# Kernel optimization log

Measured on AMD Instinct MI355X. Metric: run time of the kernel, lower is better.

The kernel has to match this reference:

```python
import jax, jax.numpy as jnp
import numpy as np

ALPHA = 0.2  # LeakyReLU negative slope (init arg alpha)


def setup_inputs() -> dict:
    key = jax.random.key(0)
    k1, k2, k3 = jax.random.split(key, 3)
    B, N, F_in, F_out = 8, 2048, 256, 256
    inp = jax.random.normal(k1, (B, N, F_in), dtype=jnp.float32)
    adj = jnp.ones((B, N, N), dtype=jnp.float32)  # unused by the module's forward
    # xavier_uniform with gain=1.414
    gain = 1.414
    bW = gain * np.sqrt(6.0 / (F_in + F_out))
    W = jax.random.uniform(k2, (F_in, F_out), minval=-bW, maxval=bW, dtype=jnp.float32)
    ba = gain * np.sqrt(6.0 / (2 * F_out + 1))
    a = jax.random.uniform(k3, (2 * F_out, 1), minval=-ba, maxval=ba, dtype=jnp.float32)
    return {"inp": inp, "adj": adj, "W": W, "a": a}


def reference(inp, adj, W, a):
    # inp: [B, N, F_in]; W: [F_in, F_out]; a: [2*F_out, 1]. adj is unused (as in source).
    F_out = W.shape[1]
    h = jnp.matmul(inp, W)  # [B, N, F_out]
    # e[b,i,j] = leakyrelu(a1 . h_i + a2 . h_j)  (equivalent to the repeat+cat+matmul)
    a1 = a[:F_out, 0]
    a2 = a[F_out:, 0]
    s1 = jnp.einsum('bnf,f->bn', h, a1)  # [B, N]
    s2 = jnp.einsum('bnf,f->bn', h, a2)  # [B, N]
    e = jax.nn.leaky_relu(s1[:, :, None] + s2[:, None, :], negative_slope=ALPHA)  # [B, N, N]
    # global per-batch min-max normalization, then affine *30 - 20
    mn = jnp.min(e, axis=(1, 2), keepdims=True)
    mx = jnp.max(e, axis=(1, 2), keepdims=True)
    e = (e - mn) / (mx - mn) * 30.0 - 20.0
    attention = jax.nn.sigmoid(e)  # dropout p=0 / eval: identity
    h_prime = jnp.matmul(attention, h)  # [B, N, F_out]
    h_prime = jax.nn.elu(h_prime)  # concat=True branch
    return h_prime, attention
```

## Files before the change

kernel.cpp:

```cpp
#include <hip/hip_runtime.h>
#include <stdint.h>

#define B_   8
#define N_   2048
#define F_   256
#define BN_  (B_ * N_)
#define ALPHA_ 0.2f

typedef __attribute__((ext_vector_type(8))) short  short8;
typedef __attribute__((ext_vector_type(4))) float  f32x4;

__device__ __forceinline__ unsigned short f2bf(float x) {
  uint32_t u = __float_as_uint(x);
  uint32_t r = (u + 0x7fffu + ((u >> 16) & 1u)) >> 16;
  return (unsigned short)r;
}

__device__ __forceinline__ uint32_t fkey(float f) {
  uint32_t b = __float_as_uint(f);
  return b ^ (uint32_t)(((int32_t)b >> 31) | (int32_t)0x80000000);
}
__device__ __forceinline__ float ikey(uint32_t k) {
  uint32_t b = (k & 0x80000000u) ? (k ^ 0x80000000u) : ~k;
  return __uint_as_float(b);
}

__device__ __forceinline__ void async_load16(const void* g, void* l) {
  __builtin_amdgcn_global_load_lds(
      (const __attribute__((address_space(1))) uint32_t*)g,
      (__attribute__((address_space(3))) uint32_t*)l, 16, 0, 0);
}

__device__ __forceinline__ void nt_store4(float* p, f32x4 v) {
  __builtin_nontemporal_store(v, (f32x4*)p);
}

__global__ void k_cvt_w(const float* __restrict__ W, unsigned short* __restrict__ WT) {
  int k = blockIdx.x, n = threadIdx.x;
  WT[n * F_ + k] = f2bf(W[k * F_ + n]);
}

__launch_bounds__(256, 1)
__global__ void k_gemm1(const float* __restrict__ inp,
                        const unsigned short* __restrict__ WT,
                        const float* __restrict__ avec,
                        unsigned short* __restrict__ hT,
                        float* __restrict__ s1g, float* __restrict__ s2g,
                        uint32_t* __restrict__ maxk, uint32_t* __restrict__ mink) {
  __shared__ __align__(16) unsigned short Atile[64 * 32];
  __shared__ __align__(16) unsigned short Btile[256 * 32];
  __shared__ __align__(16) unsigned short Trans[256 * 72];
  __shared__ float s1_lds[64], s2_lds[64];

  const int tid  = threadIdx.x;
  const int wave = tid >> 6, lane = tid & 63;
  const int n16  = lane & 15, quad = lane >> 4;
  const int i0   = blockIdx.x * 64;
  const int b    = i0 >> 11;

  if (tid < 64) { s1_lds[tid] = 0.0f; s2_lds[tid] = 0.0f; }

  f32x4 acc[4][4];
  #pragma unroll
  for (int mt = 0; mt < 4; ++mt)
    #pragma unroll
    for (int nt = 0; nt < 4; ++nt) acc[mt][nt] = (f32x4){0.f, 0.f, 0.f, 0.f};

  for (int k0 = 0; k0 < F_; k0 += 32) {
    {
      int r = tid >> 2, cp = tid & 3;
      const float* gp = inp + (size_t)(i0 + r) * F_ + k0 + cp * 8;
      float4 va = *(const float4*)gp;
      float4 vb = *(const float4*)(gp + 4);
      short8 sv;
      sv[0] = (short)f2bf(va.x); sv[1] = (short)f2bf(va.y);
      sv[2] = (short)f2bf(va.z); sv[3] = (short)f2bf(va.w);
      sv[4] = (short)f2bf(vb.x); sv[5] = (short)f2bf(vb.y);
      sv[6] = (short)f2bf(vb.z); sv[7] = (short)f2bf(vb.w);
      *(short8*)((char*)Atile + r * 64 + cp * 16) = sv;
    }
    #pragma unroll
    for (int g4 = 0; g4 < 4; ++g4) {
      int f = (wave << 6) + (g4 << 4) + (lane >> 2);
      int p = lane & 3;
      async_load16(WT + (size_t)f * F_ + k0 + p * 8,
                   (char*)Btile + wave * 4096 + g4 * 1024);
    }
    __syncthreads();

    short8 af[4], bf_[4];
    #pragma unroll
    for (int mt = 0; mt < 4; ++mt)
      af[mt] = *(const short8*)((const char*)Atile + ((mt * 16 + n16) * 64 + quad * 16));
    #pragma unroll
    for (int nt = 0; nt < 4; ++nt)
      bf_[nt] = *(const short8*)((const char*)Btile + ((wave * 64 + nt * 16 + n16) * 64 + quad * 16));
    #pragma unroll
    for (int mt = 0; mt < 4; ++mt)
      #pragma unroll
      for (int nt = 0; nt < 4; ++nt)
        acc[mt][nt] = __builtin_amdgcn_mfma_f32_16x16x32_bf16(af[mt], bf_[nt], acc[mt][nt], 0, 0, 0);
    __syncthreads();
  }

  #pragma unroll
  for (int mt = 0; mt < 4; ++mt)
    #pragma unroll
    for (int nt = 0; nt < 4; ++nt) {
      int f = (wave << 6) + (nt << 4) + n16;
      int i = (mt << 4) + (quad << 2);
      ushort4 pk;
      pk.x = f2bf(acc[mt][nt][0]); pk.y = f2bf(acc[mt][nt][1]);
      pk.z = f2bf(acc[mt][nt][2]); pk.w = f2bf(acc[mt][nt][3]);
      *(ushort4*)(Trans + f * 72 + i) = pk;
    }

  float a1v[4], a2v[4];
  #pragma unroll
  for (int nt = 0; nt < 4; ++nt) {
    int f = (wave << 6) + (nt << 4) + n16;
    a1v[nt] = avec[f];
    a2v[nt] = avec[F_ + f];
  }
  #pragma unroll
  for (int mt = 0; mt < 4; ++mt) {
    float s1p[4] = {0, 0, 0, 0}, s2p[4] = {0, 0, 0, 0};
    #pragma unroll
    for (int nt = 0; nt < 4; ++nt)
      #pragma unroll
      for (int rg = 0; rg < 4; ++rg) {
        s1p[rg] = fmaf(acc[mt][nt][rg], a1v[nt], s1p[rg]);
        s2p[rg] = fmaf(acc[mt][nt][rg], a2v[nt], s2p[rg]);
      }
    #pragma unroll
    for (int rg = 0; rg < 4; ++rg) {
      float v1 = s1p[rg], v2 = s2p[rg];
      #pragma unroll
      for (int off = 1; off < 16; off <<= 1) {
        v1 += __shfl_xor(v1, off);
        v2 += __shfl_xor(v2, off);
      }
      if (n16 == 0) {
        atomicAdd(&s1_lds[(mt << 4) + (quad << 2) + rg], v1);
        atomicAdd(&s2_lds[(mt << 4) + (quad << 2) + rg], v2);
      }
    }
  }
  __syncthreads();

  #pragma unroll
  for (int it = 0; it < 8; ++it) {
    int f = it * 32 + wave * 8 + (lane >> 3);
    int i = (lane & 7) * 8;
    short8 v = *(const short8*)(Trans + f * 72 + i);
    *(short8*)(hT + (size_t)f * BN_ + i0 + i) = v;
  }

  if (tid < 64) {
    float v1 = s1_lds[tid], v2 = s2_lds[tid];
    s1g[i0 + tid] = v1;
    s2g[i0 + tid] = v2;
    float mn1 = v1, mx1 = v1, mn2 = v2, mx2 = v2;
    #pragma unroll
    for (int off = 1; off < 64; off <<= 1) {
      mn1 = fminf(mn1, __shfl_xor(mn1, off));
      mx1 = fmaxf(mx1, __shfl_xor(mx1, off));
      mn2 = fminf(mn2, __shfl_xor(mn2, off));
      mx2 = fmaxf(mx2, __shfl_xor(mx2, off));
    }
    if (tid == 0) {
      atomicMax(&maxk[b * 2 + 0], fkey(mx1));
      atomicMax(&maxk[b * 2 + 1], fkey(mx2));
      atomicMin(&mink[b * 2 + 0], fkey(mn1));
      atomicMin(&mink[b * 2 + 1], fkey(mn2));
    }
  }
}

__launch_bounds__(256, 2)
__global__ void k_gemm2(const unsigned short* __restrict__ hT,
                        const float* __restrict__ s1, const float* __restrict__ s2,
                        const uint32_t* __restrict__ maxk, const uint32_t* __restrict__ mink,
                        float* __restrict__ hprime,
                        float* __restrict__ att) {
  __shared__ __align__(16) unsigned short Btile[2][256 * 32];
  __shared__ __align__(16) unsigned short Atile[2][1024];
  __shared__ __align__(16) float s2_lds[N_];

  const int tid  = threadIdx.x;
  const int wave = tid >> 6, lane = tid & 63;
  const int n16  = lane & 15, quad = lane >> 4;
  const int blk  = blockIdx.x;
  const int b    = blk & 7;
  const int i0   = (blk >> 3) * 32;

  float mx1 = ikey(maxk[b * 2 + 0]), mx2 = ikey(maxk[b * 2 + 1]);
  float mn1 = ikey(mink[b * 2 + 0]), mn2 = ikey(mink[b * 2 + 1]);
  float smn = mn1 + mn2, smx = mx1 + mx2;
  float emn = fmaxf(smn, ALPHA_ * smn);
  float emx = fmaxf(smx, ALPHA_ * smx);
  float scale  = 30.0f / (emx - emn);
  const float uscale = -scale;
  const float ubias  = emn * scale + 20.0f;

  const int r_att = tid >> 3;
  const int c_att = tid & 7;
  const float s1v = s1[b * N_ + i0 + r_att];
  const float* s2b = s2 + b * N_;
  float* attrow = att + ((size_t)(b * N_ + i0 + r_att)) * N_;

  auto stage_b = [&](int buf_, int k0_) {
    #pragma unroll
    for (int g4 = 0; g4 < 4; ++g4) {
      int f = (wave << 6) + (g4 << 4) + (lane >> 2);
      int p = lane & 3;
      async_load16(hT + (size_t)f * BN_ + b * N_ + k0_ + p * 8,
                   (char*)Btile + buf_ * 16384 + wave * 4096 + g4 * 1024);
    }
  };

  #pragma unroll
  for (int it = 0; it < 2; ++it)
    async_load16(s2b + wave * 512 + it * 256 + lane * 4,
                 (char*)s2_lds + wave * 2048 + it * 1024);
  stage_b(0, 0);
  asm volatile("s_waitcnt vmcnt(0) lgkmcnt(0)" ::: "memory");
  __builtin_amdgcn_s_barrier();
  asm volatile("" ::: "memory");

  f32x4 acc[2][4];
  #pragma unroll
  for (int mt = 0; mt < 2; ++mt)
    #pragma unroll
    for (int nt = 0; nt < 4; ++nt) acc[mt][nt] = (f32x4){0.f, 0.f, 0.f, 0.f};

  for (int t = 0; t < 64; ++t) {
    const int cur = t & 1;
    const int k0  = t << 5;

    float4 va = *(const float4*)((const char*)s2_lds + k0 * 4 + c_att * 16);
    float v[4] = {va.x, va.y, va.z, va.w};
    #pragma unroll
    for (int jj = 0; jj < 4; ++jj) {
      float s = s1v + v[jj];
      float l = fmaxf(s, ALPHA_ * s);
      float u = fmaf(l, uscale, ubias);
      float p_ = __builtin_amdgcn_rcpf(1.0f + __expf(u));
      v[jj] = p_;
    }
    nt_store4(attrow + k0 + c_att * 4, (f32x4){v[0], v[1], v[2], v[3]});
    ushort4 spk;
    spk.x = f2bf(v[0]); spk.y = f2bf(v[1]); spk.z = f2bf(v[2]); spk.w = f2bf(v[3]);
    *(ushort4*)((char*)Atile + cur * 2048 + tid * 8) = spk;

    asm volatile("s_waitcnt vmcnt(1) lgkmcnt(0)" ::: "memory");
    __builtin_amdgcn_s_barrier();
    asm volatile("" ::: "memory");

    short8 af0 = *(const short8*)((const char*)Atile + cur * 2048 + n16 * 64 + quad * 16);
    short8 af1 = *(const short8*)((const char*)Atile + cur * 2048 + (16 + n16) * 64 + quad * 16);
    short8 bf_[4];
    #pragma unroll
    for (int nt = 0; nt < 4; ++nt)
      bf_[nt] = *(const short8*)((const char*)Btile + cur * 16384 +
                                 (wave * 64 + nt * 16 + n16) * 64 + quad * 16);

    if (t < 63) stage_b(cur ^ 1, k0 + 32);

    #pragma unroll
    for (int nt = 0; nt < 4; ++nt) {
      acc[0][nt] = __builtin_amdgcn_mfma_f32_16x16x32_bf16(af0, bf_[nt], acc[0][nt], 0, 0, 0);
      acc[1][nt] = __builtin_amdgcn_mfma_f32_16x16x32_bf16(af1, bf_[nt], acc[1][nt], 0, 0, 0);
    }
  }

  float* hp = hprime + ((size_t)(b * N_ + i0)) * F_;
  #pragma unroll
  for (int mt = 0; mt < 2; ++mt)
    #pragma unroll
    for (int nt = 0; nt < 4; ++nt) {
      int fcol = (wave << 6) + (nt << 4) + n16;
      int irow = (mt << 4) + (quad << 2);
      #pragma unroll
      for (int rg = 0; rg < 4; ++rg) {
        float x = acc[mt][nt][rg];
        float y = x > 0.0f ? x : (__expf(x) - 1.0f);
        __builtin_nontemporal_store(y, hp + (size_t)(irow + rg) * F_ + fcol);
      }
    }
}

extern "C" void kernel_launch(void* const* d_in, const int* in_sizes, int n_in,
                              void* d_out, int out_size, void* d_ws, size_t ws_size,
                              hipStream_t stream) {
  const float* inp  = (const float*)d_in[0];
  const float* W    = (const float*)d_in[2];
  const float* avec = (const float*)d_in[3];

  float* hprime = (float*)d_out;
  float* att    = (float*)d_out + (size_t)B_ * N_ * F_;

  char* ws = (char*)d_ws;
  unsigned short* WT = (unsigned short*)ws;
  unsigned short* hT = (unsigned short*)(ws + 131072);
  float* s1          = (float*)(ws + 131072 + 8388608);
  float* s2          = s1 + BN_;
  uint32_t* maxk     = (uint32_t*)(s2 + BN_);
  uint32_t* mink     = maxk + 16;

  (void)hipMemsetAsync(maxk, 0x00, 64, stream);
  (void)hipMemsetAsync(mink, 0xFF, 64, stream);

  k_cvt_w<<<F_, F_, 0, stream>>>(W, WT);
  k_gemm1<<<BN_ / 64, 256, 0, stream>>>(inp, WT, avec, hT, s1, s2, maxk, mink);
  k_gemm2<<<512, 256, 0, stream>>>(hT, s1, s2, maxk, mink, hprime, att);
}
```

Baseline: 269.1 us.

## Triple-buffer gemm2 B tiles, alias gemm1 LDS, fold memsets into weight conversion

The attention GEMM kernel now keeps three B-tile buffers with a prefetch distance of two iterations, issued right after the barrier, with adjusted vmcnt waits. The first GEMM reuses one LDS region for staging tiles and the transpose buffer, allowing two blocks per CU. The min/max key reset moves from two memset calls into the weight conversion kernel. The last iterations issue prefetches past the needed range, which read unused memory.

New measurement: 272.7 us. Within noise of the previous version (+1.3%).

```diff
diff --git a/kernel.cpp b/kernel.cpp
--- a/kernel.cpp
+++ b/kernel.cpp
@@ -35,22 +35,24 @@
   __builtin_nontemporal_store(v, (f32x4*)p);
 }
 
-__global__ void k_cvt_w(const float* __restrict__ W, unsigned short* __restrict__ WT) {
+__global__ void k_cvt_w(const float* __restrict__ W, unsigned short* __restrict__ WT,
+                        uint32_t* __restrict__ maxk, uint32_t* __restrict__ mink) {
   int k = blockIdx.x, n = threadIdx.x;
+  if (k == 0 && n < 16) { maxk[n] = 0u; mink[n] = 0xFFFFFFFFu; }
   WT[n * F_ + k] = f2bf(W[k * F_ + n]);
 }
 
-__launch_bounds__(256, 1)
+__launch_bounds__(256, 2)
 __global__ void k_gemm1(const float* __restrict__ inp,
                         const unsigned short* __restrict__ WT,
                         const float* __restrict__ avec,
                         unsigned short* __restrict__ hT,
                         float* __restrict__ s1g, float* __restrict__ s2g,
                         uint32_t* __restrict__ maxk, uint32_t* __restrict__ mink) {
-  __shared__ __align__(16) unsigned short Atile[64 * 32];
-  __shared__ __align__(16) unsigned short Btile[256 * 32];
-  __shared__ __align__(16) unsigned short Trans[256 * 72];
+  __shared__ __align__(16) char smem[256 * 72 * 2];
   __shared__ float s1_lds[64], s2_lds[64];
+  unsigned short* Atile = (unsigned short*)smem;
+  unsigned short* Btile = (unsigned short*)(smem + 4096);
 
   const int tid  = threadIdx.x;
   const int wave = tid >> 6, lane = tid & 63;
@@ -103,6 +105,8 @@
     __syncthreads();
   }
 
+  unsigned short* Trans = (unsigned short*)smem;
+
   #pragma unroll
   for (int mt = 0; mt < 4; ++mt)
     #pragma unroll
@@ -183,7 +187,7 @@
                         const uint32_t* __restrict__ maxk, const uint32_t* __restrict__ mink,
                         float* __restrict__ hprime,
                         float* __restrict__ att) {
-  __shared__ __align__(16) unsigned short Btile[2][256 * 32];
+  __shared__ __align__(16) unsigned short Btile[3][256 * 32];
   __shared__ __align__(16) unsigned short Atile[2][1024];
   __shared__ __align__(16) float s2_lds[N_];
 
@@ -209,13 +213,13 @@
   const float* s2b = s2 + b * N_;
   float* attrow = att + ((size_t)(b * N_ + i0 + r_att)) * N_;
 
-  auto stage_b = [&](int buf_, int k0_) {
+  auto stage_b = [&](int slot, int k0_) {
     #pragma unroll
     for (int g4 = 0; g4 < 4; ++g4) {
       int f = (wave << 6) + (g4 << 4) + (lane >> 2);
       int p = lane & 3;
       async_load16(hT + (size_t)f * BN_ + b * N_ + k0_ + p * 8,
-                   (char*)Btile + buf_ * 16384 + wave * 4096 + g4 * 1024);
+                   (char*)Btile + slot * 16384 + wave * 4096 + g4 * 1024);
     }
   };
 
@@ -224,7 +228,8 @@
     async_load16(s2b + wave * 512 + it * 256 + lane * 4,
                  (char*)s2_lds + wave * 2048 + it * 1024);
   stage_b(0, 0);
-  asm volatile("s_waitcnt vmcnt(0) lgkmcnt(0)" ::: "memory");
+  stage_b(1, 32);
+  asm volatile("s_waitcnt vmcnt(8)" ::: "memory");
   __builtin_amdgcn_s_barrier();
   asm volatile("" ::: "memory");
 
@@ -234,9 +239,10 @@
     #pragma unroll
     for (int nt = 0; nt < 4; ++nt) acc[mt][nt] = (f32x4){0.f, 0.f, 0.f, 0.f};
 
+  int sl_r = 0, sl_n = 2;
   for (int t = 0; t < 64; ++t) {
-    const int cur = t & 1;
-    const int k0  = t << 5;
+    const int abuf = (t & 1) * 2048;
+    const int k0   = t << 5;
 
     float4 va = *(const float4*)((const char*)s2_lds + k0 * 4 + c_att * 16);
     float v[4] = {va.x, va.y, va.z, va.w};
@@ -251,28 +257,33 @@
     nt_store4(attrow + k0 + c_att * 4, (f32x4){v[0], v[1], v[2], v[3]});
     ushort4 spk;
     spk.x = f2bf(v[0]); spk.y = f2bf(v[1]); spk.z = f2bf(v[2]); spk.w = f2bf(v[3]);
-    *(ushort4*)((char*)Atile + cur * 2048 + tid * 8) = spk;
-
-    asm volatile("s_waitcnt vmcnt(1) lgkmcnt(0)" ::: "memory");
+    *(ushort4*)((char*)Atile + abuf + tid * 8) = spk;
+
+    asm volatile("s_waitcnt vmcnt(5) lgkmcnt(0)" ::: "memory");
     __builtin_amdgcn_s_barrier();
     asm volatile("" ::: "memory");
 
-    short8 af0 = *(const short8*)((const char*)Atile + cur * 2048 + n16 * 64 + quad * 16);
-    short8 af1 = *(const short8*)((const char*)Atile + cur * 2048 + (16 + n16) * 64 + quad * 16);
+    stage_b(sl_n, k0 + 64);
+
+    short8 af0 = *(const short8*)((const char*)Atile + abuf + n16 * 64 + quad * 16);
+    short8 af1 = *(const short8*)((const char*)Atile + abuf + (16 + n16) * 64 + quad * 16);
     short8 bf_[4];
     #pragma unroll
     for (int nt = 0; nt < 4; ++nt)
-      bf_[nt] = *(const short8*)((const char*)Btile + cur * 16384 +
+      bf_[nt] = *(const short8*)((const char*)Btile + sl_r * 16384 +
                                  (wave * 64 + nt * 16 + n16) * 64 + quad * 16);
-
-    if (t < 63) stage_b(cur ^ 1, k0 + 32);
 
     #pragma unroll
     for (int nt = 0; nt < 4; ++nt) {
       acc[0][nt] = __builtin_amdgcn_mfma_f32_16x16x32_bf16(af0, bf_[nt], acc[0][nt], 0, 0, 0);
       acc[1][nt] = __builtin_amdgcn_mfma_f32_16x16x32_bf16(af1, bf_[nt], acc[1][nt], 0, 0, 0);
     }
-  }
+
+    sl_r = (sl_r == 2) ? 0 : sl_r + 1;
+    sl_n = (sl_n == 2) ? 0 : sl_n + 1;
+  }
+
+  asm volatile("s_waitcnt vmcnt(0)" ::: "memory");
 
   float* hp = hprime + ((size_t)(b * N_ + i0)) * F_;
   #pragma unroll
@@ -308,10 +319,7 @@
   uint32_t* maxk     = (uint32_t*)(s2 + BN_);
   uint32_t* mink     = maxk + 16;
 
-  (void)hipMemsetAsync(maxk, 0x00, 64, stream);
-  (void)hipMemsetAsync(mink, 0xFF, 64, stream);
-
-  k_cvt_w<<<F_, F_, 0, stream>>>(W, WT);
+  k_cvt_w<<<F_, F_, 0, stream>>>(W, WT, maxk, mink);
   k_gemm1<<<BN_ / 64, 256, 0, stream>>>(inp, WT, avec, hT, s1, s2, maxk, mink);
   k_gemm2<<<512, 256, 0, stream>>>(hT, s1, s2, maxk, mink, hprime, att);
 }
```
